# Kernel optimization log

Hardware: AMD Instinct MI355X
Metric: run time of the kernel (lower is better)

The kernel has to match this reference:

```python
import jax, jax.numpy as jnp
import numpy as np

D = 256  # hardcoded Dense units in the original layer

def setup_inputs() -> dict:
    key = jax.random.key(0)
    ks = jax.random.split(key, 7)
    B, S, F = 8, 2048, 256
    x = jax.random.normal(ks[0], (B, S, F), dtype=jnp.float32)
    # Dense layers (kernel + bias), glorot-ish scale
    scale = 1.0 / np.sqrt(F)
    Wq = jax.random.normal(ks[1], (F, D), dtype=jnp.float32) * scale
    Wk = jax.random.normal(ks[2], (F, D), dtype=jnp.float32) * scale
    Wv = jax.random.normal(ks[3], (F, D), dtype=jnp.float32) * scale
    bq = jax.random.normal(ks[4], (D,), dtype=jnp.float32) * 0.01
    bk = jax.random.normal(ks[5], (D,), dtype=jnp.float32) * 0.01
    bv = jax.random.normal(ks[6], (D,), dtype=jnp.float32) * 0.01
    return {"x": x, "Wq": Wq, "bq": bq, "Wk": Wk, "bk": bk, "Wv": Wv, "bv": bv}

def reference(x, Wq, bq, Wk, bk, Wv, bv):
    # Q/K/V projections: Dense(256) == x @ W + b
    Q = jnp.einsum('bsf,fd->bsd', x, Wq) + bq
    K = jnp.einsum('bsf,fd->bsd', x, Wk) + bk
    V = jnp.einsum('bsf,fd->bsd', x, Wv) + bv
    scores = jnp.einsum('bqd,bkd->bqk', Q, K) / jnp.sqrt(jnp.float32(D))
    attn = jax.nn.softmax(scores, axis=-1)
    return jnp.einsum('bqk,bkd->bqd', attn, V)
```

## Files before the change

kernel.cpp:

```cpp
#include <hip/hip_runtime.h>

typedef __bf16 bf16;
typedef __bf16 bf16x4v __attribute__((ext_vector_type(4)));
typedef __bf16 bf16x8 __attribute__((ext_vector_type(8)));
typedef float f32x4 __attribute__((ext_vector_type(4)));
typedef short s16x4 __attribute__((ext_vector_type(4)));

#define MFMA_X32(A, B, C) __builtin_amdgcn_mfma_f32_16x16x32_bf16(A, B, C, 0, 0, 0)

#if __has_builtin(__builtin_amdgcn_mfma_f32_16x16x16_bf16)
static __device__ __forceinline__ f32x4 mfma_x16(bf16x4v a, bf16x4v b, f32x4 c) {
  return __builtin_amdgcn_mfma_f32_16x16x16_bf16(a, b, c, 0, 0, 0);
}
#else
static __device__ __forceinline__ f32x4 mfma_x16(bf16x4v a, bf16x4v b, f32x4 c) {
  return __builtin_amdgcn_mfma_f32_16x16x16bf16_1k(
      __builtin_bit_cast(s16x4, a), __builtin_bit_cast(s16x4, b), c, 0, 0, 0);
}
#endif

static __device__ __forceinline__ float fast_exp2(float x) {
  float r;
  asm volatile("v_exp_f32 %0, %1\n\ts_nop 0" : "=v"(r) : "v"(x));
  return r;
}

static __device__ __forceinline__ void gll16(const void* g, void* l) {
  __builtin_amdgcn_global_load_lds(
      (const __attribute__((address_space(1))) void*)g,
      (__attribute__((address_space(3))) void*)l, 16, 0, 0);
}

#define WT_OFF 0
#define Q_OFF 393216
#define K_OFF 8781824
#define V_OFF 17170432

__global__ __launch_bounds__(256) void prep_wt(const float* __restrict__ Wq,
                                               const float* __restrict__ Wk,
                                               const float* __restrict__ Wv,
                                               bf16* __restrict__ Wt) {
  const int idx = blockIdx.x * 256 + threadIdx.x;
  const int p = idx >> 16;
  const int rem = idx & 65535;
  const int k = rem >> 8, n = rem & 255;
  const float* W = (p == 0) ? Wq : ((p == 1) ? Wk : Wv);
  Wt[p * 65536 + n * 256 + k] = (bf16)W[rem];
}

__global__ __launch_bounds__(256, 3) void proj_qkv(const float* __restrict__ x,
                                                   const float* __restrict__ bq,
                                                   const float* __restrict__ bk,
                                                   const float* __restrict__ bv,
                                                   char* __restrict__ ws0) {
  __shared__ __align__(16) bf16 xs[32][264];
  __shared__ __align__(16) bf16 wth[64][264];
  const bf16* Wt = (const bf16*)(ws0 + WT_OFF);
  bf16* Qo = (bf16*)(ws0 + Q_OFF);
  bf16* Ko = (bf16*)(ws0 + K_OFF);
  bf16* Vc = (bf16*)(ws0 + V_OFF);
  const int t = threadIdx.x;
  const int rowbase = blockIdx.x * 32;

  {
    const int rr = t >> 6, c4 = (t & 63) * 4;
#pragma unroll
    for (int i = 0; i < 8; ++i) {
      const int r = i * 4 + rr;
      const float4 v = *(const float4*)&x[(rowbase + r) * 256 + c4];
      bf16x4v h;
      h[0] = (bf16)v.x; h[1] = (bf16)v.y; h[2] = (bf16)v.z; h[3] = (bf16)v.w;
      *(bf16x4v*)&xs[r][c4] = h;
    }
  }
  __syncthreads();
  const int lane = t & 63, w = t >> 6, l16 = lane & 15, quad = lane >> 4;
  const int rsub = (w & 1) * 16, csub = (w >> 1) * 32;

  bf16x8 a[8];
#pragma unroll
  for (int kt = 0; kt < 8; ++kt)
    a[kt] = *(const bf16x8*)&xs[rsub + l16][kt * 32 + quad * 8];

  for (int p = 0; p < 3; ++p) {
    const float* bias = (p == 0) ? bq : ((p == 1) ? bk : bv);
    const float sc = (p == 0) ? 0.09016844005556021f : 1.0f;
    for (int q = 0; q < 4; ++q) {
      __syncthreads();
#pragma unroll
      for (int i = 0; i < 8; ++i) {
        const int u = i * 256 + t;
        const int row = u >> 5, c8 = (u & 31) * 8;
        *(bf16x8*)&wth[row][c8] =
            *(const bf16x8*)&Wt[p * 65536 + (q * 64 + row) * 256 + c8];
      }
      __syncthreads();
      f32x4 acc[2] = {f32x4{0.f, 0.f, 0.f, 0.f}, f32x4{0.f, 0.f, 0.f, 0.f}};
#pragma unroll
      for (int kt = 0; kt < 8; ++kt)
#pragma unroll
        for (int nt = 0; nt < 2; ++nt) {
          const bf16x8 bfr =
              *(const bf16x8*)&wth[csub + nt * 16 + l16][kt * 32 + quad * 8];
          acc[nt] = MFMA_X32(a[kt], bfr, acc[nt]);
        }
#pragma unroll
      for (int nt = 0; nt < 2; ++nt) {
        const int n = q * 64 + csub + nt * 16 + l16;
        const float bb = bias[n];
#pragma unroll
        for (int r = 0; r < 4; ++r) {
          const int row = rowbase + rsub + quad * 4 + r;
          const bf16 hv = (bf16)((acc[nt][r] + bb) * sc);
          if (p == 0) {
            Qo[row * 256 + n] = hv;
          } else {
            const int b2 = row >> 11, s = row & 2047;
            if (p == 1)
              Ko[b2 * 524288 + (s >> 4) * 4096 + (n >> 5) * 512 +
                 ((n >> 3) & 3) * 128 + (s & 15) * 8 + (n & 7)] = hv;
            else
              Vc[b2 * 524288 + (s >> 4) * 4096 + (n >> 4) * 256 +
                 (((s & 15) >> 2)) * 64 + (n & 15) * 4 + (s & 3)] = hv;
          }
        }
      }
    }
  }
}

#define BUF_SZ 65536
#define SLOT_SZ 16640

__global__ __launch_bounds__(512, 2) void flash_attn(const char* __restrict__ ws0,
                                                     float* __restrict__ out) {
  __shared__ __align__(1024) char smem[135168];
  const bf16* Qp = (const bf16*)(ws0 + Q_OFF);
  const int t = threadIdx.x;
  const int lane = t & 63, w = t >> 6;
  const int l16 = lane & 15, quad = lane >> 4;
  const int qs = w & 1, kq = w >> 1;
  const int b = blockIdx.x & 7;
  const int qt = blockIdx.x >> 3;
  const int qrow0 = b * 2048 + qt * 64 + qs * 32;

  bf16x8 qf[2][8];
#pragma unroll
  for (int qsub = 0; qsub < 2; ++qsub)
#pragma unroll
    for (int kt = 0; kt < 8; ++kt)
      qf[qsub][kt] =
          *(const bf16x8*)&Qp[(qrow0 + qsub * 16 + l16) * 256 + kt * 32 + quad * 8];

  f32x4 o[2][16];
#pragma unroll
  for (int qsub = 0; qsub < 2; ++qsub)
#pragma unroll
    for (int dt = 0; dt < 16; ++dt) o[qsub][dt] = f32x4{0.f, 0.f, 0.f, 0.f};
  float m_[2] = {-1e30f, -1e30f}, l_[2] = {0.f, 0.f};

  unsigned goff[8], loff[8];
#pragma unroll
  for (int i = 0; i < 8; ++i) {
    const int u = w * 8 + i;
    const int kq2 = (u & 31) >> 3, e = u & 7;
    goff[i] = (u < 32 ? (unsigned)K_OFF : (unsigned)V_OFF) + b * 1048576u +
              kq2 * 262144u + e * 1024u + lane * 16u;
    loff[i] = kq2 * 16384u + (u < 32 ? 0u : 8192u) + e * 1024u;
  }
#pragma unroll
  for (int i = 0; i < 8; ++i) gll16(ws0 + goff[i], smem + loff[i]);

  for (int it = 0; it < 32; ++it) {
    __syncthreads();
    const unsigned cur = (unsigned)(it & 1) * BUF_SZ;
    if (it + 1 < 32) {
      const unsigned nxt = (unsigned)((it + 1) & 1) * BUF_SZ;
      const unsigned gadd = (unsigned)(it + 1) * 8192u;
#pragma unroll
      for (int i = 0; i < 8; ++i) gll16(ws0 + goff[i] + gadd, smem + nxt + loff[i]);
    }

    const char* kb = smem + cur + kq * 16384 + lane * 16;
    f32x4 s0 = f32x4{0.f, 0.f, 0.f, 0.f}, s1 = s0;
#pragma unroll
    for (int kt = 0; kt < 8; ++kt) {
      const bf16x8 kf = *(const bf16x8*)(kb + kt * 1024);
      s0 = MFMA_X32(kf, qf[0][kt], s0);
      s1 = MFMA_X32(kf, qf[1][kt], s1);
    }

    bf16x4v pa[2];
#pragma unroll
    for (int qsub = 0; qsub < 2; ++qsub) {
      const f32x4 s = qsub ? s1 : s0;
      float cm = fmaxf(fmaxf(s[0], s[1]), fmaxf(s[2], s[3]));
      cm = fmaxf(cm, __shfl_xor(cm, 16));
      cm = fmaxf(cm, __shfl_xor(cm, 32));
      const float mold = m_[qsub];
      const float mnew = fmaxf(mold, cm);
      bf16x4v pp;
      float ps = 0.f;
#pragma unroll
      for (int r = 0; r < 4; ++r) {
        const float e = fast_exp2(s[r] - mnew);
        const bf16 pb = (bf16)e;
        pp[r] = pb;
        ps += (float)pb;
      }
      ps += __shfl_xor(ps, 16);
      ps += __shfl_xor(ps, 32);
      if (__any(mnew > mold)) {
        const float al = fast_exp2(mold - mnew);
        m_[qsub] = mnew;
        l_[qsub] = l_[qsub] * al + ps;
        float ar[4];
#pragma unroll
        for (int r = 0; r < 4; ++r)
          ar[r] = __shfl(al, (quad << 4) + (quad << 2) + r);
#pragma unroll
        for (int dt = 0; dt < 16; ++dt)
#pragma unroll
          for (int r = 0; r < 4; ++r) o[qsub][dt][r] *= ar[r];
      } else {
        l_[qsub] += ps;
      }
      pa[qsub] = pp;
    }

    const char* vb = smem + cur + kq * 16384 + 8192 + lane * 8;
#pragma unroll
    for (int dt = 0; dt < 16; ++dt) {
      const bf16x4v vf = *(const bf16x4v*)(vb + dt * 512);
      o[0][dt] = mfma_x16(pa[0], vf, o[0][dt]);
      o[1][dt] = mfma_x16(pa[1], vf, o[1][dt]);
    }
  }

  float* mlf = (float*)(smem + 133120);
  if (quad == 0) {
#pragma unroll
    for (int qsub = 0; qsub < 2; ++qsub) {
      const int base = ((kq * 2 + qs) * 2 + qsub) * 32;
      mlf[base + l16] = m_[qsub];
      mlf[base + 16 + l16] = l_[qsub];
    }
  }
  __syncthreads();
#pragma unroll
  for (int qsub = 0; qsub < 2; ++qsub) {
    float M = -1e30f, mk[4], lk[4];
#pragma unroll
    for (int k2 = 0; k2 < 4; ++k2) {
      const int base = ((k2 * 2 + qs) * 2 + qsub) * 32;
      mk[k2] = mlf[base + l16];
      lk[k2] = mlf[base + 16 + l16];
      M = fmaxf(M, mk[k2]);
    }
    float L = 0.f;
#pragma unroll
    for (int k2 = 0; k2 < 4; ++k2) L += lk[k2] * fast_exp2(mk[k2] - M);
    const float sg = fast_exp2(m_[qsub] - M) / L;
    float sr[4];
#pragma unroll
    for (int r = 0; r < 4; ++r) sr[r] = __shfl(sg, (quad << 4) + (quad << 2) + r);
#pragma unroll
    for (int dt = 0; dt < 16; ++dt)
#pragma unroll
      for (int r = 0; r < 4; ++r) o[qsub][dt][r] *= sr[r];
  }
  if (kq >= 2) {
#pragma unroll
    for (int qsub = 0; qsub < 2; ++qsub) {
      float* sb = (float*)(smem + ((kq - 2) * 4 + qs * 2 + qsub) * SLOT_SZ);
#pragma unroll
      for (int dt = 0; dt < 16; ++dt)
#pragma unroll
        for (int r = 0; r < 4; ++r)
          sb[(quad * 4 + r) * 260 + dt * 16 + l16] = o[qsub][dt][r];
    }
  }
  __syncthreads();
  if (kq < 2) {
#pragma unroll
    for (int qsub = 0; qsub < 2; ++qsub) {
      const float* sb = (const float*)(smem + (kq * 4 + qs * 2 + qsub) * SLOT_SZ);
#pragma unroll
      for (int dt = 0; dt < 16; ++dt)
#pragma unroll
        for (int r = 0; r < 4; ++r)
          o[qsub][dt][r] += sb[(quad * 4 + r) * 260 + dt * 16 + l16];
    }
  }
  __syncthreads();
  if (kq == 1) {
#pragma unroll
    for (int qsub = 0; qsub < 2; ++qsub) {
      float* sb = (float*)(smem + (qs * 2 + qsub) * SLOT_SZ);
#pragma unroll
      for (int dt = 0; dt < 16; ++dt)
#pragma unroll
        for (int r = 0; r < 4; ++r)
          sb[(quad * 4 + r) * 260 + dt * 16 + l16] = o[qsub][dt][r];
    }
  }
  __syncthreads();
  if (kq == 0) {
#pragma unroll
    for (int qsub = 0; qsub < 2; ++qsub) {
      const float* sb = (const float*)(smem + (qs * 2 + qsub) * SLOT_SZ);
#pragma unroll
      for (int dt = 0; dt < 16; ++dt)
#pragma unroll
        for (int r = 0; r < 4; ++r) {
          const float v = o[qsub][dt][r] + sb[(quad * 4 + r) * 260 + dt * 16 + l16];
          out[(qrow0 + qsub * 16 + quad * 4 + r) * 256 + dt * 16 + l16] = v;
        }
    }
  }
}

extern "C" void kernel_launch(void* const* d_in, const int* in_sizes, int n_in,
                              void* d_out, int out_size, void* d_ws,
                              size_t ws_size, hipStream_t stream) {
  const float* x = (const float*)d_in[0];
  const float* Wq = (const float*)d_in[1];
  const float* bq = (const float*)d_in[2];
  const float* Wk = (const float*)d_in[3];
  const float* bk = (const float*)d_in[4];
  const float* Wv = (const float*)d_in[5];
  const float* bv = (const float*)d_in[6];
  float* out = (float*)d_out;
  char* ws = (char*)d_ws;

  prep_wt<<<768, 256, 0, stream>>>(Wq, Wk, Wv, (bf16*)(ws + WT_OFF));
  proj_qkv<<<512, 256, 0, stream>>>(x, bq, bk, bv, ws);
  flash_attn<<<256, 512, 0, stream>>>(ws, out);
}
```

Before: 178.0 us.

## Restructure QKV projection: weights in registers, double-buffered x tiles, LDS-staged coalesced stores

The projection kernel is reorganised so that each block owns one 128-column chunk of one of Q, K or V. That chunk's weight fragments are held in registers for the whole block, and the block streams four 32-row tiles of x through double-buffered, XOR-swizzled LDS, prefetching the next tile into registers. Outputs are first assembled in LDS in the target layout, then written to global memory as contiguous 16-byte stores instead of scattered 2-byte stores. The cost is that x is now read six times across blocks instead of once, plus higher register pressure from the weight fragments.

```diff
diff --git a/kernel.cpp b/kernel.cpp
--- a/kernel.cpp
+++ b/kernel.cpp
@@ -53,80 +53,132 @@
                                                    const float* __restrict__ bk,
                                                    const float* __restrict__ bv,
                                                    char* __restrict__ ws0) {
-  __shared__ __align__(16) bf16 xs[32][264];
-  __shared__ __align__(16) bf16 wth[64][264];
+  __shared__ __align__(16) char smem[40960];
   const bf16* Wt = (const bf16*)(ws0 + WT_OFF);
   bf16* Qo = (bf16*)(ws0 + Q_OFF);
   bf16* Ko = (bf16*)(ws0 + K_OFF);
   bf16* Vc = (bf16*)(ws0 + V_OFF);
   const int t = threadIdx.x;
-  const int rowbase = blockIdx.x * 32;
-
-  {
-    const int rr = t >> 6, c4 = (t & 63) * 4;
-#pragma unroll
-    for (int i = 0; i < 8; ++i) {
-      const int r = i * 4 + rr;
-      const float4 v = *(const float4*)&x[(rowbase + r) * 256 + c4];
-      bf16x4v h;
-      h[0] = (bf16)v.x; h[1] = (bf16)v.y; h[2] = (bf16)v.z; h[3] = (bf16)v.w;
-      *(bf16x4v*)&xs[r][c4] = h;
-    }
-  }
-  __syncthreads();
   const int lane = t & 63, w = t >> 6, l16 = lane & 15, quad = lane >> 4;
-  const int rsub = (w & 1) * 16, csub = (w >> 1) * 32;
-
-  bf16x8 a[8];
-#pragma unroll
-  for (int kt = 0; kt < 8; ++kt)
-    a[kt] = *(const bf16x8*)&xs[rsub + l16][kt * 32 + quad * 8];
-
-  for (int p = 0; p < 3; ++p) {
-    const float* bias = (p == 0) ? bq : ((p == 1) ? bk : bv);
-    const float sc = (p == 0) ? 0.09016844005556021f : 1.0f;
-    for (int q = 0; q < 4; ++q) {
-      __syncthreads();
-#pragma unroll
-      for (int i = 0; i < 8; ++i) {
-        const int u = i * 256 + t;
-        const int row = u >> 5, c8 = (u & 31) * 8;
-        *(bf16x8*)&wth[row][c8] =
-            *(const bf16x8*)&Wt[p * 65536 + (q * 64 + row) * 256 + c8];
+  const int fam = blockIdx.x % 6;
+  const int rgroup = blockIdx.x / 6;
+  const int p = fam >> 1, ch = fam & 1;
+  const float* bias = (p == 0) ? bq : ((p == 1) ? bk : bv);
+  const float sc = (p == 0) ? 0.09016844005556021f : 1.0f;
+
+  const int nl = w * 32 + l16;
+  bf16x8 bfr[2][8];
+#pragma unroll
+  for (int nt = 0; nt < 2; ++nt)
+#pragma unroll
+    for (int kt = 0; kt < 8; ++kt)
+      bfr[nt][kt] = *(const bf16x8*)&Wt[p * 65536 + (ch * 128 + nl + nt * 16) * 256 +
+                                        kt * 32 + quad * 8];
+  float bias2[2];
+#pragma unroll
+  for (int nt = 0; nt < 2; ++nt) bias2[nt] = bias[ch * 128 + nl + nt * 16];
+
+  const int row0 = rgroup * 128;
+  char* outL = smem + 32768;
+
+  float4 xr[4][2];
+#define STAGE_LOAD(tile)                                                        \
+  {                                                                             \
+    const float* xp = x + (row0 + (tile) * 32) * 256;                           \
+    _Pragma("unroll") for (int i = 0; i < 4; ++i) {                             \
+      const int u2 = i * 256 + t, row = u2 >> 5, col8 = (u2 & 31) * 8;          \
+      xr[i][0] = *(const float4*)&xp[row * 256 + col8];                         \
+      xr[i][1] = *(const float4*)&xp[row * 256 + col8 + 4];                     \
+    }                                                                           \
+  }
+#define STAGE_WRITE(buf)                                                        \
+  {                                                                             \
+    _Pragma("unroll") for (int i = 0; i < 4; ++i) {                             \
+      const int u2 = i * 256 + t, row = u2 >> 5, col8 = (u2 & 31) * 8;          \
+      const float* f0 = (const float*)&xr[i][0];                                \
+      const float* f1 = (const float*)&xr[i][1];                                \
+      bf16x8 h;                                                                 \
+      _Pragma("unroll") for (int j = 0; j < 4; ++j) {                           \
+        h[j] = (bf16)f0[j];                                                     \
+        h[4 + j] = (bf16)f1[j];                                                 \
+      }                                                                         \
+      *(bf16x8*)&smem[(buf) * 16384 + row * 512 +                               \
+                      ((col8 * 2) ^ ((row & 7) << 4))] = h;                     \
+    }                                                                           \
+  }
+
+  STAGE_LOAD(0);
+  STAGE_WRITE(0);
+  __syncthreads();
+
+  int cur = 0;
+  for (int tt = 0; tt < 4; ++tt) {
+    if (tt < 3) STAGE_LOAD(tt + 1);
+
+    f32x4 acc[2][2];
+#pragma unroll
+    for (int rs = 0; rs < 2; ++rs)
+#pragma unroll
+      for (int nt = 0; nt < 2; ++nt) acc[rs][nt] = f32x4{0.f, 0.f, 0.f, 0.f};
+    const char* xb = smem + cur * 16384;
+#pragma unroll
+    for (int rs = 0; rs < 2; ++rs) {
+      const int row = rs * 16 + l16;
+#pragma unroll
+      for (int kt = 0; kt < 8; ++kt) {
+        const bf16x8 a = *(const bf16x8*)(xb + row * 512 +
+                                          ((kt * 64 + quad * 16) ^ ((l16 & 7) << 4)));
+        acc[rs][0] = MFMA_X32(a, bfr[0][kt], acc[rs][0]);
+        acc[rs][1] = MFMA_X32(a, bfr[1][kt], acc[rs][1]);
       }
-      __syncthreads();
-      f32x4 acc[2] = {f32x4{0.f, 0.f, 0.f, 0.f}, f32x4{0.f, 0.f, 0.f, 0.f}};
-#pragma unroll
-      for (int kt = 0; kt < 8; ++kt)
-#pragma unroll
-        for (int nt = 0; nt < 2; ++nt) {
-          const bf16x8 bfr =
-              *(const bf16x8*)&wth[csub + nt * 16 + l16][kt * 32 + quad * 8];
-          acc[nt] = MFMA_X32(a[kt], bfr, acc[nt]);
+    }
+    __syncthreads();
+
+#pragma unroll
+    for (int rs = 0; rs < 2; ++rs)
+#pragma unroll
+      for (int nt = 0; nt < 2; ++nt)
+#pragma unroll
+        for (int r = 0; r < 4; ++r) {
+          const int sl = rs * 16 + quad * 4 + r;
+          const int nn = nl + nt * 16;
+          const bf16 hv = (bf16)((acc[rs][nt][r] + bias2[nt]) * sc);
+          int pos;
+          if (p == 0)
+            pos = sl * 128 + nn;
+          else if (p == 1)
+            pos = (sl >> 4) * 2048 + (nn >> 5) * 512 + ((nn >> 3) & 3) * 128 +
+                  (sl & 15) * 8 + (nn & 7);
+          else
+            pos = (sl >> 4) * 2048 + (nn >> 4) * 256 + ((sl & 15) >> 2) * 64 +
+                  (nn & 15) * 4 + (sl & 3);
+          *(bf16*)(outL + pos * 2) = hv;
         }
-#pragma unroll
-      for (int nt = 0; nt < 2; ++nt) {
-        const int n = q * 64 + csub + nt * 16 + l16;
-        const float bb = bias[n];
-#pragma unroll
-        for (int r = 0; r < 4; ++r) {
-          const int row = rowbase + rsub + quad * 4 + r;
-          const bf16 hv = (bf16)((acc[nt][r] + bb) * sc);
-          if (p == 0) {
-            Qo[row * 256 + n] = hv;
-          } else {
-            const int b2 = row >> 11, s = row & 2047;
-            if (p == 1)
-              Ko[b2 * 524288 + (s >> 4) * 4096 + (n >> 5) * 512 +
-                 ((n >> 3) & 3) * 128 + (s & 15) * 8 + (n & 7)] = hv;
-            else
-              Vc[b2 * 524288 + (s >> 4) * 4096 + (n >> 4) * 256 +
-                 (((s & 15) >> 2)) * 64 + (n & 15) * 4 + (s & 3)] = hv;
-          }
-        }
-      }
-    }
-  }
+    if (tt < 3) STAGE_WRITE(cur ^ 1);
+    __syncthreads();
+
+    const int rowg = row0 + tt * 32;
+    if (p == 0) {
+      const int row = t >> 3, cb = (t & 7) * 32;
+      const float4 v0 = *(const float4*)(outL + row * 256 + cb);
+      const float4 v1 = *(const float4*)(outL + row * 256 + cb + 16);
+      char* dst = (char*)Qo + (rowg + row) * 512 + ch * 256 + cb;
+      *(float4*)dst = v0;
+      *(float4*)(dst + 16) = v1;
+    } else {
+      const int b2 = rowg >> 11, s0 = rowg & 2047;
+      bf16* O = (p == 1) ? Ko : Vc;
+      char* dst = (char*)O + b2 * 1048576 + ((s0 >> 4) + (t >> 7)) * 8192 +
+                  ch * 4096 + (t & 127) * 32;
+      const float4 v0 = *(const float4*)(outL + t * 32);
+      const float4 v1 = *(const float4*)(outL + t * 32 + 16);
+      *(float4*)dst = v0;
+      *(float4*)(dst + 16) = v1;
+    }
+    cur ^= 1;
+  }
+#undef STAGE_LOAD
+#undef STAGE_WRITE
 }
 
 #define BUF_SZ 65536
@@ -334,6 +386,6 @@
   char* ws = (char*)d_ws;
 
   prep_wt<<<768, 256, 0, stream>>>(Wq, Wk, Wv, (bf16*)(ws + WT_OFF));
-  proj_qkv<<<512, 256, 0, stream>>>(x, bq, bk, bv, ws);
+  proj_qkv<<<768, 256, 0, stream>>>(x, bq, bk, bv, ws);
   flash_attn<<<256, 512, 0, stream>>>(ws, out);
 }
```

Result: no change. 177.2 us (-0.5%).
